# Optimization experiments

Hardware: AMD Instinct MI355X
Metric: run time of the kernel (lower is better)

Reference implementation:

```python
import jax, jax.numpy as jnp
import numpy as np
import math

D_MODEL = 1024
H = 16
D_K = D_MODEL // H
B = 4
S = 2048
NEG = -1e9


def setup_inputs() -> dict:
    key = jax.random.key(0)
    ks = jax.random.split(key, 11)
    scale = 1.0 / math.sqrt(D_MODEL)
    inp = {
        'q': jax.random.normal(ks[0], (B, S, D_MODEL), dtype=jnp.float32),
        'k': jax.random.normal(ks[1], (B, S, D_MODEL), dtype=jnp.float32),
        'v': jax.random.normal(ks[2], (B, S, D_MODEL), dtype=jnp.float32),
        'wq': jax.random.normal(ks[3], (D_MODEL, D_MODEL), dtype=jnp.float32) * scale,
        'bq': jnp.zeros((D_MODEL,), dtype=jnp.float32),
        'wk': jax.random.normal(ks[4], (D_MODEL, D_MODEL), dtype=jnp.float32) * scale,
        'bk': jnp.zeros((D_MODEL,), dtype=jnp.float32),
        'wv': jax.random.normal(ks[5], (D_MODEL, D_MODEL), dtype=jnp.float32) * scale,
        'bv': jnp.zeros((D_MODEL,), dtype=jnp.float32),
        'wo': jax.random.normal(ks[6], (D_MODEL, D_MODEL), dtype=jnp.float32) * scale,
        'bo': jnp.zeros((D_MODEL,), dtype=jnp.float32),
        # broadcastable causal mask [1, 1, S, S]; 0 = masked out
        'mask': jnp.tril(jnp.ones((S, S), dtype=jnp.int32))[None, None, :, :],
    }
    return inp


def reference(q, k, v, wq, bq, wk, bk, wv, bv, wo, bo, mask):
    # QKV projections: x @ W^T + b (nn.Linear convention)
    def split_heads(x):  # [B, S, D] -> [B, H, S, d_k]
        return x.reshape(B, S, H, D_K).transpose(0, 2, 1, 3)

    query = split_heads(q @ wq.T + bq)
    key_ = split_heads(k @ wk.T + bk)
    value = split_heads(v @ wv.T + bv)

    # scaled dot-product attention with mask; scores: [B, H, S, S]
    scores = jnp.einsum('bhqd,bhkd->bhqk', query, key_) / math.sqrt(D_K)
    scores = jnp.where(mask == 0, jnp.float32(NEG), scores)
    attn = jax.nn.softmax(scores, axis=-1)
    ctx = jnp.einsum('bhqk,bhkd->bhqd', attn, value)  # [B, H, S, d_k]

    # merge heads and output projection
    ctx = ctx.transpose(0, 2, 1, 3).reshape(B, S, D_MODEL)
    return ctx @ wo.T + bo
```

## Files before the change

kernel.cpp:

```cpp
#include <hip/hip_runtime.h>

#define DEVI __device__ __forceinline__

typedef __attribute__((ext_vector_type(8))) __bf16 bf16x8;
typedef __attribute__((ext_vector_type(4))) float f32x4;

DEVI __bf16 f2bf(float f) {
  unsigned u = __builtin_bit_cast(unsigned, f);
  unsigned r = u + 0x7fffu + ((u >> 16) & 1u);
  unsigned short h = (unsigned short)(r >> 16);
  return __builtin_bit_cast(__bf16, h);
}

DEVI unsigned cvt_pk_bf16(float lo, float hi) {
  unsigned r;
  asm("v_cvt_pk_bf16_f32 %0, %1, %2" : "=v"(r) : "v"(lo), "v"(hi));
  return r;
}

DEVI void load_lds16(const void* g, void* l) {
  __builtin_amdgcn_global_load_lds((__attribute__((address_space(1))) const void*)g,
                                   (__attribute__((address_space(3))) void*)l,
                                   16, 0, 0);
}

__global__ void convert_bf16(const float* __restrict__ in, __bf16* __restrict__ out, int n8) {
  int stride = gridDim.x * blockDim.x;
  for (int i = blockIdx.x * blockDim.x + threadIdx.x; i < n8; i += stride) {
    float4 a = ((const float4*)in)[i * 2];
    float4 b = ((const float4*)in)[i * 2 + 1];
    bf16x8 o;
    o[0] = f2bf(a.x); o[1] = f2bf(a.y); o[2] = f2bf(a.z); o[3] = f2bf(a.w);
    o[4] = f2bf(b.x); o[5] = f2bf(b.y); o[6] = f2bf(b.z); o[7] = f2bf(b.w);
    ((bf16x8*)out)[i] = o;
  }
}

template<int MODE>
__global__ __launch_bounds__(256, 2) void gemm_bt(
    const __bf16* __restrict__ A, const __bf16* __restrict__ W,
    const float* __restrict__ bias, void* __restrict__ outp)
{
  __shared__ __bf16 As[2][128 * 32];
  __shared__ __bf16 Bs[2][128 * 32];
  const int tid = threadIdx.x;
  const int lane = tid & 63;
  const int ln = lane & 15, g = lane >> 4;
  const int w = tid >> 6;
  const int wr = w >> 1, wc = w & 1;
  const int row0 = blockIdx.x * 128, col0 = blockIdx.y * 128;

  f32x4 acc[4][4] = {};

  auto stage = [&](int buf, int k0) {
#pragma unroll
    for (int i = 0; i < 2; ++i) {
      int c = tid + 256 * i;
      int r = c >> 2, ko = (c & 3) * 8;
      load_lds16(&A[(size_t)(row0 + r) * 1024 + k0 + ko], &As[buf][c * 8]);
      load_lds16(&W[(size_t)(col0 + r) * 1024 + k0 + ko], &Bs[buf][c * 8]);
    }
  };

  stage(0, 0);
#pragma unroll 2
  for (int kt = 0; kt < 32; ++kt) {
    __syncthreads();
    if (kt + 1 < 32) stage((kt + 1) & 1, (kt + 1) * 32);
    const __bf16* as = As[kt & 1];
    const __bf16* bs = Bs[kt & 1];
    bf16x8 aF[4], bF[4];
#pragma unroll
    for (int mi = 0; mi < 4; ++mi)
      aF[mi] = *(const bf16x8*)&as[(wr * 64 + mi * 16 + ln) * 32 + g * 8];
#pragma unroll
    for (int ni = 0; ni < 4; ++ni)
      bF[ni] = *(const bf16x8*)&bs[(wc * 64 + ni * 16 + ln) * 32 + g * 8];
#pragma unroll
    for (int mi = 0; mi < 4; ++mi)
#pragma unroll
      for (int ni = 0; ni < 4; ++ni)
        acc[mi][ni] = __builtin_amdgcn_mfma_f32_16x16x32_bf16(aF[mi], bF[ni], acc[mi][ni], 0, 0, 0);
  }

#pragma unroll
  for (int ni = 0; ni < 4; ++ni) {
    int n = col0 + wc * 64 + ni * 16 + ln;
    float bv = bias[n];
#pragma unroll
    for (int mi = 0; mi < 4; ++mi) {
#pragma unroll
      for (int i = 0; i < 4; ++i) {
        int m = row0 + wr * 64 + mi * 16 + g * 4 + i;
        float val = acc[mi][ni][i] + bv;
        if (MODE == 2) {
          ((float*)outp)[(size_t)m * 1024 + n] = val;
        } else {
          int b = m >> 11, s = m & 2047, h = n >> 6, d = n & 63;
          size_t idx = (MODE == 0)
            ? ((size_t)((b * 16 + h) * 2048 + s) * 64 + d)
            : ((size_t)((b * 16 + h) * 64 + d) * 2048 + s);
          ((__bf16*)outp)[idx] = f2bf(val);
        }
      }
    }
  }
}

__global__ __launch_bounds__(256, 3) void attn_fwd(
    const __bf16* __restrict__ Qh, const __bf16* __restrict__ Kh,
    const __bf16* __restrict__ Vt, __bf16* __restrict__ Ctx)
{
  __shared__ __bf16 Ks[2][64 * 64];
  __shared__ __bf16 Vs[2][64 * 64];
  __shared__ __align__(16) char Pbuf[4][2][2048];

  const int tid = threadIdx.x;
  const int lane = tid & 63;
  const int ln = lane & 15, g = lane >> 4;
  const int w = tid >> 6;
  const int bh = blockIdx.x;
  const int q0 = (int)(gridDim.y - 1 - blockIdx.y) * 128;
  const int qw = q0 + w * 32;
  const float CE = 0.18033688f;

  bf16x8 qF[2][2];
#pragma unroll
  for (int qt = 0; qt < 2; ++qt)
#pragma unroll
    for (int ksb = 0; ksb < 2; ++ksb)
      qF[qt][ksb] = *(const bf16x8*)&Qh[((size_t)bh * 2048 + qw + qt * 16 + ln) * 64 + ksb * 32 + g * 8];

  f32x4 oT[2][4] = {};
  float mrun[2] = {-3e38f, -3e38f}, lrun[2] = {0.f, 0.f};

  const int nt = q0 / 64 + 2;

  auto stageKV = [&](int buf, int t) {
    int kv0 = t * 64;
#pragma unroll
    for (int i = 0; i < 2; ++i) {
      int c = tid + 256 * i;
      int r = c >> 3, sl = c & 7;
      int so = 8 * (sl ^ (r & 7));
      load_lds16(&Kh[((size_t)bh * 2048 + kv0 + r) * 64 + so], &Ks[buf][c * 8]);
      load_lds16(&Vt[((size_t)bh * 64 + r) * 2048 + kv0 + so], &Vs[buf][c * 8]);
    }
  };

  stageKV(0, 0);
  for (int t = 0; t < nt; ++t) {
    __syncthreads();
    if (t + 1 < nt) stageKV((t + 1) & 1, t + 1);
    const int kv0 = t * 64;
    if (kv0 > qw + 31) continue;
    const __bf16* ksm = Ks[t & 1];
    const __bf16* vsm = Vs[t & 1];
    const bool need_mask = (kv0 + 63 > qw);

    f32x4 sT[2][4] = {};
#pragma unroll
    for (int ksb = 0; ksb < 2; ++ksb) {
      bf16x8 aK[4];
#pragma unroll
      for (int ni = 0; ni < 4; ++ni) {
        int r = ni * 16 + ln;
        aK[ni] = *(const bf16x8*)&ksm[r * 64 + ((ksb * 32 + g * 8) ^ ((r & 7) * 8))];
      }
#pragma unroll
      for (int qt = 0; qt < 2; ++qt)
#pragma unroll
        for (int ni = 0; ni < 4; ++ni)
          sT[qt][ni] = __builtin_amdgcn_mfma_f32_16x16x32_bf16(aK[ni], qF[qt][ksb], sT[qt][ni], 0, 0, 0);
    }

#pragma unroll
    for (int qt = 0; qt < 2; ++qt) {
      const int qglob = qw + qt * 16 + ln;
      if (need_mask) {
#pragma unroll
        for (int ni = 0; ni < 4; ++ni)
#pragma unroll
          for (int i = 0; i < 4; ++i) {
            int kvg = kv0 + ni * 16 + 4 * g + i;
            sT[qt][ni][i] = (kvg <= qglob) ? sT[qt][ni][i] : -3e38f;
          }
      }
      f32x4 vm0, vm1;
#pragma unroll
      for (int i = 0; i < 4; ++i) {
        vm0[i] = fmaxf(sT[qt][0][i], sT[qt][1][i]);
        vm1[i] = fmaxf(sT[qt][2][i], sT[qt][3][i]);
      }
      float mx = fmaxf(fmaxf(fmaxf(vm0[0], vm0[1]), fmaxf(vm0[2], vm0[3])),
                       fmaxf(fmaxf(vm1[0], vm1[1]), fmaxf(vm1[2], vm1[3])));
      mx = fmaxf(mx, __shfl_xor(mx, 16));
      mx = fmaxf(mx, __shfl_xor(mx, 32));
      float mnew = fmaxf(mrun[qt], mx);
      float fac = exp2f((mrun[qt] - mnew) * CE);
      mrun[qt] = mnew;
      float psum = 0.f;
      char* pw = Pbuf[w][qt];
#pragma unroll
      for (int ni = 0; ni < 4; ++ni) {
        float p0 = exp2f((sT[qt][ni][0] - mnew) * CE);
        float p1 = exp2f((sT[qt][ni][1] - mnew) * CE);
        float p2 = exp2f((sT[qt][ni][2] - mnew) * CE);
        float p3 = exp2f((sT[qt][ni][3] - mnew) * CE);
        psum += (p0 + p1) + (p2 + p3);
        unsigned d0 = cvt_pk_bf16(p0, p1);
        unsigned d1 = cvt_pk_bf16(p2, p3);
        *(uint2*)(pw + ln * 128 + ((32 * ni + 8 * g) ^ ((ln & 7) << 4))) = make_uint2(d0, d1);
      }
      lrun[qt] = lrun[qt] * fac + psum;
#pragma unroll
      for (int di = 0; di < 4; ++di)
#pragma unroll
        for (int i = 0; i < 4; ++i)
          oT[qt][di][i] *= fac;
    }

    asm volatile("" ::: "memory");

#pragma unroll
    for (int ksb = 0; ksb < 2; ++ksb) {
      bf16x8 aV[4], bP[2];
#pragma unroll
      for (int di = 0; di < 4; ++di) {
        int r = di * 16 + ln;
        aV[di] = *(const bf16x8*)&vsm[r * 64 + ((ksb * 32 + g * 8) ^ ((r & 7) * 8))];
      }
#pragma unroll
      for (int qt = 0; qt < 2; ++qt)
        bP[qt] = *(const bf16x8*)(Pbuf[w][qt] + ln * 128 + ((64 * ksb + 16 * g) ^ ((ln & 7) << 4)));
#pragma unroll
      for (int qt = 0; qt < 2; ++qt)
#pragma unroll
        for (int di = 0; di < 4; ++di)
          oT[qt][di] = __builtin_amdgcn_mfma_f32_16x16x32_bf16(aV[di], bP[qt], oT[qt][di], 0, 0, 0);
    }
  }

  const int b = bh >> 4, h = bh & 15;
#pragma unroll
  for (int qt = 0; qt < 2; ++qt) {
    float lr = lrun[qt];
    lr += __shfl_xor(lr, 16);
    lr += __shfl_xor(lr, 32);
    float inv = 1.0f / lr;
    int qrow = qw + qt * 16 + ln;
#pragma unroll
    for (int di = 0; di < 4; ++di) {
      unsigned o01 = cvt_pk_bf16(oT[qt][di][0] * inv, oT[qt][di][1] * inv);
      unsigned o23 = cvt_pk_bf16(oT[qt][di][2] * inv, oT[qt][di][3] * inv);
      size_t idx = ((size_t)(b * 2048 + qrow)) * 1024 + h * 64 + di * 16 + 4 * g;
      *(uint2*)&Ctx[idx] = make_uint2(o01, o23);
    }
  }
}

extern "C" void kernel_launch(void* const* d_in, const int* in_sizes, int n_in,
                              void* d_out, int out_size, void* d_ws, size_t ws_size,
                              hipStream_t stream) {
  const float* q  = (const float*)d_in[0];
  const float* k  = (const float*)d_in[1];
  const float* v  = (const float*)d_in[2];
  const float* wq = (const float*)d_in[3];
  const float* bq = (const float*)d_in[4];
  const float* wk = (const float*)d_in[5];
  const float* bk = (const float*)d_in[6];
  const float* wv = (const float*)d_in[7];
  const float* bv = (const float*)d_in[8];
  const float* wo = (const float*)d_in[9];
  const float* bo = (const float*)d_in[10];
  float* out = (float*)d_out;
  char* ws = (char*)d_ws;

  const size_t MB = 1024 * 1024;
  __bf16* Wqb  = (__bf16*)(ws + 0 * MB);
  __bf16* Wkb  = (__bf16*)(ws + 2 * MB);
  __bf16* Wvb  = (__bf16*)(ws + 4 * MB);
  __bf16* Wob  = (__bf16*)(ws + 6 * MB);
  __bf16* Abuf = (__bf16*)(ws + 8 * MB);
  __bf16* Qh   = (__bf16*)(ws + 24 * MB);
  __bf16* Kh   = (__bf16*)(ws + 40 * MB);
  __bf16* Vt   = (__bf16*)(ws + 56 * MB);
  __bf16* Ctx  = Abuf;

  const int W8 = 1024 * 1024 / 8;
  const int X8 = 8192 * 1024 / 8;
  auto cgrid = [](int n8) { int nb = (n8 + 255) / 256; return dim3((unsigned)(nb < 2048 ? nb : 2048)); };

  convert_bf16<<<cgrid(W8), 256, 0, stream>>>(wq, Wqb, W8);
  convert_bf16<<<cgrid(W8), 256, 0, stream>>>(wk, Wkb, W8);
  convert_bf16<<<cgrid(W8), 256, 0, stream>>>(wv, Wvb, W8);
  convert_bf16<<<cgrid(W8), 256, 0, stream>>>(wo, Wob, W8);

  dim3 ggrid(64, 8);
  convert_bf16<<<cgrid(X8), 256, 0, stream>>>(q, Abuf, X8);
  gemm_bt<0><<<ggrid, 256, 0, stream>>>(Abuf, Wqb, bq, Qh);
  convert_bf16<<<cgrid(X8), 256, 0, stream>>>(k, Abuf, X8);
  gemm_bt<0><<<ggrid, 256, 0, stream>>>(Abuf, Wkb, bk, Kh);
  convert_bf16<<<cgrid(X8), 256, 0, stream>>>(v, Abuf, X8);
  gemm_bt<1><<<ggrid, 256, 0, stream>>>(Abuf, Wvb, bv, Vt);

  attn_fwd<<<dim3(64, 16), 256, 0, stream>>>(Qh, Kh, Vt, Ctx);
  gemm_bt<2><<<ggrid, 256, 0, stream>>>(Ctx, Wob, bo, out);
}
```

Measured before the change: 235.0 us.

## Switch attention to 32x32x16 MFMA with register-resident P and lazy rescaling

Rewrites the attention inner loop to use 32x32x16 bf16 MFMAs, one 32-row query tile per wave. The softmax probabilities are now passed to the PV MFMA through cross-lane shuffles instead of a round trip through an LDS P buffer. The running max is only updated and the accumulators rescaled when some lane's new max exceeds the old one by a threshold, which cuts the rescale multiplies. Query blocks are launched in an interleaved order to balance the causal workload. The lazy-max threshold lets exponentials exceed 1, adding some risk of overflow or lost bf16 precision.

```diff
diff --git a/kernel.cpp b/kernel.cpp
--- a/kernel.cpp
+++ b/kernel.cpp
@@ -4,6 +4,8 @@
 
 typedef __attribute__((ext_vector_type(8))) __bf16 bf16x8;
 typedef __attribute__((ext_vector_type(4))) float f32x4;
+typedef __attribute__((ext_vector_type(16))) float f32x16;
+typedef __attribute__((ext_vector_type(4))) unsigned uint32x4;
 
 DEVI __bf16 f2bf(float f) {
   unsigned u = __builtin_bit_cast(unsigned, f);
@@ -113,26 +115,26 @@
 {
   __shared__ __bf16 Ks[2][64 * 64];
   __shared__ __bf16 Vs[2][64 * 64];
-  __shared__ __align__(16) char Pbuf[4][2][2048];
 
   const int tid = threadIdx.x;
   const int lane = tid & 63;
-  const int ln = lane & 15, g = lane >> 4;
+  const int l31 = lane & 31, hl = lane >> 5;
   const int w = tid >> 6;
   const int bh = blockIdx.x;
-  const int q0 = (int)(gridDim.y - 1 - blockIdx.y) * 128;
+  const int yy = blockIdx.y;
+  const int qb = (yy & 1) ? (yy >> 1) : (15 - (yy >> 1));
+  const int q0 = qb * 128;
   const int qw = q0 + w * 32;
+  const int qglob = qw + l31;
   const float CE = 0.18033688f;
 
-  bf16x8 qF[2][2];
-#pragma unroll
-  for (int qt = 0; qt < 2; ++qt)
-#pragma unroll
-    for (int ksb = 0; ksb < 2; ++ksb)
-      qF[qt][ksb] = *(const bf16x8*)&Qh[((size_t)bh * 2048 + qw + qt * 16 + ln) * 64 + ksb * 32 + g * 8];
-
-  f32x4 oT[2][4] = {};
-  float mrun[2] = {-3e38f, -3e38f}, lrun[2] = {0.f, 0.f};
+  bf16x8 qF[4];
+#pragma unroll
+  for (int ds = 0; ds < 4; ++ds)
+    qF[ds] = *(const bf16x8*)&Qh[((size_t)bh * 2048 + qglob) * 64 + ds * 16 + hl * 8];
+
+  f32x16 oT[2] = {};
+  float mrun = -3e38f, lrun = 0.f;
 
   const int nt = q0 / 64 + 2;
 
@@ -156,107 +158,105 @@
     if (kv0 > qw + 31) continue;
     const __bf16* ksm = Ks[t & 1];
     const __bf16* vsm = Vs[t & 1];
-    const bool need_mask = (kv0 + 63 > qw);
-
-    f32x4 sT[2][4] = {};
-#pragma unroll
-    for (int ksb = 0; ksb < 2; ++ksb) {
+
+    f32x16 sT[2] = {};
+#pragma unroll
+    for (int kblk = 0; kblk < 2; ++kblk) {
       bf16x8 aK[4];
-#pragma unroll
-      for (int ni = 0; ni < 4; ++ni) {
-        int r = ni * 16 + ln;
-        aK[ni] = *(const bf16x8*)&ksm[r * 64 + ((ksb * 32 + g * 8) ^ ((r & 7) * 8))];
-      }
-#pragma unroll
-      for (int qt = 0; qt < 2; ++qt)
-#pragma unroll
-        for (int ni = 0; ni < 4; ++ni)
-          sT[qt][ni] = __builtin_amdgcn_mfma_f32_16x16x32_bf16(aK[ni], qF[qt][ksb], sT[qt][ni], 0, 0, 0);
-    }
-
-#pragma unroll
-    for (int qt = 0; qt < 2; ++qt) {
-      const int qglob = qw + qt * 16 + ln;
-      if (need_mask) {
-#pragma unroll
-        for (int ni = 0; ni < 4; ++ni)
-#pragma unroll
-          for (int i = 0; i < 4; ++i) {
-            int kvg = kv0 + ni * 16 + 4 * g + i;
-            sT[qt][ni][i] = (kvg <= qglob) ? sT[qt][ni][i] : -3e38f;
-          }
-      }
-      f32x4 vm0, vm1;
-#pragma unroll
-      for (int i = 0; i < 4; ++i) {
-        vm0[i] = fmaxf(sT[qt][0][i], sT[qt][1][i]);
-        vm1[i] = fmaxf(sT[qt][2][i], sT[qt][3][i]);
-      }
-      float mx = fmaxf(fmaxf(fmaxf(vm0[0], vm0[1]), fmaxf(vm0[2], vm0[3])),
-                       fmaxf(fmaxf(vm1[0], vm1[1]), fmaxf(vm1[2], vm1[3])));
-      mx = fmaxf(mx, __shfl_xor(mx, 16));
-      mx = fmaxf(mx, __shfl_xor(mx, 32));
-      float mnew = fmaxf(mrun[qt], mx);
-      float fac = exp2f((mrun[qt] - mnew) * CE);
-      mrun[qt] = mnew;
-      float psum = 0.f;
-      char* pw = Pbuf[w][qt];
-#pragma unroll
-      for (int ni = 0; ni < 4; ++ni) {
-        float p0 = exp2f((sT[qt][ni][0] - mnew) * CE);
-        float p1 = exp2f((sT[qt][ni][1] - mnew) * CE);
-        float p2 = exp2f((sT[qt][ni][2] - mnew) * CE);
-        float p3 = exp2f((sT[qt][ni][3] - mnew) * CE);
-        psum += (p0 + p1) + (p2 + p3);
-        unsigned d0 = cvt_pk_bf16(p0, p1);
-        unsigned d1 = cvt_pk_bf16(p2, p3);
-        *(uint2*)(pw + ln * 128 + ((32 * ni + 8 * g) ^ ((ln & 7) << 4))) = make_uint2(d0, d1);
-      }
-      lrun[qt] = lrun[qt] * fac + psum;
-#pragma unroll
-      for (int di = 0; di < 4; ++di)
-#pragma unroll
-        for (int i = 0; i < 4; ++i)
-          oT[qt][di][i] *= fac;
-    }
-
-    asm volatile("" ::: "memory");
-
-#pragma unroll
-    for (int ksb = 0; ksb < 2; ++ksb) {
-      bf16x8 aV[4], bP[2];
-#pragma unroll
-      for (int di = 0; di < 4; ++di) {
-        int r = di * 16 + ln;
-        aV[di] = *(const bf16x8*)&vsm[r * 64 + ((ksb * 32 + g * 8) ^ ((r & 7) * 8))];
-      }
-#pragma unroll
-      for (int qt = 0; qt < 2; ++qt)
-        bP[qt] = *(const bf16x8*)(Pbuf[w][qt] + ln * 128 + ((64 * ksb + 16 * g) ^ ((ln & 7) << 4)));
-#pragma unroll
-      for (int qt = 0; qt < 2; ++qt)
-#pragma unroll
-        for (int di = 0; di < 4; ++di)
-          oT[qt][di] = __builtin_amdgcn_mfma_f32_16x16x32_bf16(aV[di], bP[qt], oT[qt][di], 0, 0, 0);
+      const int r = kblk * 32 + l31;
+#pragma unroll
+      for (int ds = 0; ds < 4; ++ds)
+        aK[ds] = *(const bf16x8*)&ksm[r * 64 + ((ds * 16 + hl * 8) ^ ((r & 7) * 8))];
+#pragma unroll
+      for (int ds = 0; ds < 4; ++ds)
+        sT[kblk] = __builtin_amdgcn_mfma_f32_32x32x16_bf16(aK[ds], qF[ds], sT[kblk], 0, 0, 0);
+    }
+
+    if (kv0 + 63 > qw) {
+#pragma unroll
+      for (int kblk = 0; kblk < 2; ++kblk)
+#pragma unroll
+        for (int r = 0; r < 16; ++r) {
+          int kvg = kv0 + kblk * 32 + (r & 3) + 8 * (r >> 2) + 4 * hl;
+          sT[kblk][r] = (kvg <= qglob) ? sT[kblk][r] : -3e38f;
+        }
+    }
+
+    float t8[8];
+#pragma unroll
+    for (int i = 0; i < 8; ++i)
+      t8[i] = fmaxf(fmaxf(sT[0][i], sT[0][i + 8]), fmaxf(sT[1][i], sT[1][i + 8]));
+    float m4a = fmaxf(fmaxf(t8[0], t8[1]), fmaxf(t8[2], t8[3]));
+    float m4b = fmaxf(fmaxf(t8[4], t8[5]), fmaxf(t8[6], t8[7]));
+    float mx = fmaxf(m4a, m4b);
+    mx = fmaxf(mx, __shfl_xor(mx, 32));
+
+    if (__any(mx > mrun + 16.0f)) {
+      float mnew = fmaxf(mrun, mx);
+      float fac = exp2f((mrun - mnew) * CE);
+      mrun = mnew;
+      lrun *= fac;
+      oT[0] *= fac;
+      oT[1] *= fac;
+    }
+
+    const float mce = mrun * CE;
+    unsigned c0[8], c1[8];
+    float ps0 = 0.f, ps1 = 0.f, ps2 = 0.f, ps3 = 0.f;
+#pragma unroll
+    for (int w2 = 0; w2 < 8; ++w2) {
+      float p0 = exp2f(__builtin_fmaf(sT[0][2 * w2],     CE, -mce));
+      float p1 = exp2f(__builtin_fmaf(sT[0][2 * w2 + 1], CE, -mce));
+      float p2 = exp2f(__builtin_fmaf(sT[1][2 * w2],     CE, -mce));
+      float p3 = exp2f(__builtin_fmaf(sT[1][2 * w2 + 1], CE, -mce));
+      ps0 += p0; ps1 += p1; ps2 += p2; ps3 += p3;
+      c0[w2] = cvt_pk_bf16(p0, p1);
+      c1[w2] = cvt_pk_bf16(p2, p3);
+    }
+    lrun += (ps0 + ps1) + (ps2 + ps3);
+
+    uint32x4 Wv[4];
+#pragma unroll
+    for (int kblk = 0; kblk < 2; ++kblk)
+#pragma unroll
+      for (int ksl = 0; ksl < 2; ++ksl)
+#pragma unroll
+        for (int al = 0; al < 2; ++al) {
+          unsigned cp = kblk ? c1[4 * ksl + al]     : c0[4 * ksl + al];
+          unsigned cq = kblk ? c1[4 * ksl + 2 + al] : c0[4 * ksl + 2 + al];
+          unsigned cqx = __shfl_xor(cq, 32);
+          unsigned cpx = __shfl_xor(cp, 32);
+          Wv[kblk * 2 + ksl][al]     = hl ? cqx : cp;
+          Wv[kblk * 2 + ksl][al + 2] = hl ? cq  : cpx;
+        }
+
+#pragma unroll
+    for (int dblk = 0; dblk < 2; ++dblk) {
+      bf16x8 aV[4];
+      const int r = dblk * 32 + l31;
+#pragma unroll
+      for (int ks = 0; ks < 4; ++ks)
+        aV[ks] = *(const bf16x8*)&vsm[r * 64 + ((ks * 16 + hl * 8) ^ ((r & 7) * 8))];
+#pragma unroll
+      for (int ks = 0; ks < 4; ++ks)
+        oT[dblk] = __builtin_amdgcn_mfma_f32_32x32x16_bf16(
+            aV[ks], __builtin_bit_cast(bf16x8, Wv[ks]), oT[dblk], 0, 0, 0);
     }
   }
 
+  lrun += __shfl_xor(lrun, 32);
+  const float inv = 1.0f / fmaxf(lrun, 1e-30f);
   const int b = bh >> 4, h = bh & 15;
 #pragma unroll
-  for (int qt = 0; qt < 2; ++qt) {
-    float lr = lrun[qt];
-    lr += __shfl_xor(lr, 16);
-    lr += __shfl_xor(lr, 32);
-    float inv = 1.0f / lr;
-    int qrow = qw + qt * 16 + ln;
-#pragma unroll
-    for (int di = 0; di < 4; ++di) {
-      unsigned o01 = cvt_pk_bf16(oT[qt][di][0] * inv, oT[qt][di][1] * inv);
-      unsigned o23 = cvt_pk_bf16(oT[qt][di][2] * inv, oT[qt][di][3] * inv);
-      size_t idx = ((size_t)(b * 2048 + qrow)) * 1024 + h * 64 + di * 16 + 4 * g;
-      *(uint2*)&Ctx[idx] = make_uint2(o01, o23);
-    }
-  }
+  for (int dblk = 0; dblk < 2; ++dblk)
+#pragma unroll
+    for (int rb = 0; rb < 4; ++rb) {
+      unsigned u0 = cvt_pk_bf16(oT[dblk][4 * rb]     * inv, oT[dblk][4 * rb + 1] * inv);
+      unsigned u1 = cvt_pk_bf16(oT[dblk][4 * rb + 2] * inv, oT[dblk][4 * rb + 3] * inv);
+      int d = dblk * 32 + rb * 8 + 4 * hl;
+      size_t idx = ((size_t)(b * 2048 + qglob)) * 1024 + h * 64 + d;
+      *(uint2*)&Ctx[idx] = make_uint2(u0, u1);
+    }
 }
 
 extern "C" void kernel_launch(void* const* d_in, const int* in_sizes, int n_in,
```

Measured after the change: 238.2 us. About the same (+1.4%).
